# Optimization experiments

Measured on AMD Instinct MI355X. Metric: run time of the kernel, lower is better.

## Reference

```python
import math
import jax, jax.numpy as jnp
import numpy as np

B, S, D, H = 2, 2048, 1024, 16
HD = D // H

def setup_inputs() -> dict:
    key = jax.random.key(0)
    ks = jax.random.split(key, 5)
    scale = 1.0 / math.sqrt(D)
    return {
        "x": jax.random.normal(ks[0], (B, S, D), dtype=jnp.float32),
        "Wq": jax.random.normal(ks[1], (D, D), dtype=jnp.float32) * scale,
        "Wk": jax.random.normal(ks[2], (D, D), dtype=jnp.float32) * scale,
        "Wv": jax.random.normal(ks[3], (D, D), dtype=jnp.float32) * scale,
        "Wo": jax.random.normal(ks[4], (D, D), dtype=jnp.float32) * scale,
    }

def reference(x, Wq, Wk, Wv, Wo):
    b, s, d = x.shape
    # projections -> (b, h, s, hd)
    def split_heads(t):
        return t.reshape(b, s, H, HD).transpose(0, 2, 1, 3)
    q = split_heads(x @ Wq.T)
    k = split_heads(x @ Wk.T)
    v = split_heads(x @ Wv.T)
    scores = jnp.einsum('bhqd,bhkd->bhqk', q, k) / math.sqrt(HD)
    causal = jnp.tril(jnp.ones((s, s), dtype=bool))
    scores = jnp.where(causal, scores, -jnp.inf)
    weights = jax.nn.softmax(scores, axis=-1)
    attended = jnp.einsum('bhqk,bhkd->bhqd', weights, v)
    attended = attended.transpose(0, 2, 1, 3).reshape(b, s, d)
    return attended @ Wo.T
```

## Files before the change

kernel.cpp:

```cpp
#include <hip/hip_runtime.h>
#include <hip/hip_bf16.h>

#define Bb 2
#define Ss 2048
#define Dd 1024
#define Hh 16
#define HDd 64
#define Mm (Bb*Ss)

typedef __attribute__((ext_vector_type(8))) short short8;
typedef __attribute__((ext_vector_type(4))) float f32x4;

__device__ __forceinline__ unsigned short f2bf(float f) {
  unsigned int u = __float_as_uint(f);
  return (unsigned short)((u + 0x7FFFu + ((u >> 16) & 1u)) >> 16);
}

__device__ __forceinline__ void gload_lds16(const unsigned short* g, unsigned short* l) {
  __builtin_amdgcn_global_load_lds(
      (const __attribute__((address_space(1))) unsigned int*)g,
      (__attribute__((address_space(3))) unsigned int*)l, 16, 0, 0);
}

template<int ROWS>
__device__ __forceinline__ void stage_tile(const unsigned short* __restrict__ g, size_t ldg,
                                           unsigned short* s, int w, int lane) {
#pragma unroll
  for (int i = 0; i < ROWS / 32; ++i) {
    int c = (i * 4 + w) * 64 + lane;
    int row = c >> 3;
    int srcci = (lane & 7) ^ (row & 7);
    gload_lds16(g + (size_t)row * ldg + (srcci << 3), s + (i * 4 + w) * 512);
  }
}

__global__ __launch_bounds__(256) void cvt_all(
    const float* __restrict__ x,  const float* __restrict__ Wq,
    const float* __restrict__ Wk, const float* __restrict__ Wv,
    const float* __restrict__ Wo,
    unsigned short* __restrict__ xb, unsigned short* __restrict__ Wb,
    unsigned short* __restrict__ Wob) {
  int bid = blockIdx.x;
  const float* src; unsigned short* dst; int base;
  if (bid < 4096)      { src = x;  dst = xb;              base = bid; }
  else if (bid < 5120) { src = Wq; dst = Wb;              base = bid - 4096; }
  else if (bid < 6144) { src = Wk; dst = Wb + Dd * Dd;    base = bid - 5120; }
  else if (bid < 7168) { src = Wv; dst = Wb + 2 * Dd * Dd; base = bid - 6144; }
  else                 { src = Wo; dst = Wob;             base = bid - 7168; }
  int i = base * 256 + threadIdx.x;
  f32x4 v = ((const f32x4*)src)[i];
  ushort4 o;
  o.x = f2bf(v[0]); o.y = f2bf(v[1]); o.z = f2bf(v[2]); o.w = f2bf(v[3]);
  ((ushort4*)dst)[i] = o;
}

__global__ __launch_bounds__(256, 2) void gemm_qkv2(
    const unsigned short* __restrict__ xb,
    const unsigned short* __restrict__ Wb,
    unsigned short* __restrict__ Qo,
    unsigned short* __restrict__ Ko,
    unsigned short* __restrict__ Vt) {
  __shared__ unsigned short As[2][128 * 64], Bs[2][128 * 64];
  const int lin = (int)blockIdx.x + 32 * ((int)blockIdx.y + 8 * (int)blockIdx.z);
  const int orig = (lin & 7) * 96 + (lin >> 3);
  const int z = orig >> 8;
  const int rem = orig & 255;
  const int tm = (rem >> 3) * 128, tn = (rem & 7) * 128;
  const unsigned short* W = Wb + (size_t)z * Dd * Dd;
  const int tid = threadIdx.x, w = tid >> 6, lane = tid & 63;
  const int lrow = lane & 15, lgr = lane >> 4;
  const int wm = w >> 1, wn = w & 1;

  f32x4 acc[4][4] = {};
  stage_tile<128>(xb + (size_t)tm * Dd, Dd, As[0], w, lane);
  stage_tile<128>(W + (size_t)tn * Dd, Dd, Bs[0], w, lane);
  __syncthreads();
  for (int k = 0; k < 16; ++k) {
    const int cur = k & 1;
    if (k + 1 < 16) {
      stage_tile<128>(xb + (size_t)tm * Dd + (k + 1) * 64, Dd, As[cur ^ 1], w, lane);
      stage_tile<128>(W + (size_t)tn * Dd + (k + 1) * 64, Dd, Bs[cur ^ 1], w, lane);
    }
#pragma unroll
    for (int half = 0; half < 2; ++half) {
      short8 af[4], bf[4];
#pragma unroll
      for (int mt = 0; mt < 4; ++mt) {
        int row = wm * 64 + mt * 16 + lrow;
        int e = (row * 64 + half * 32 + 8 * lgr) ^ ((row & 7) << 3);
        af[mt] = *(const short8*)(As[cur] + e);
      }
#pragma unroll
      for (int nt = 0; nt < 4; ++nt) {
        int row = wn * 64 + nt * 16 + lrow;
        int e = (row * 64 + half * 32 + 8 * lgr) ^ ((row & 7) << 3);
        bf[nt] = *(const short8*)(Bs[cur] + e);
      }
      if (z != 2) {
#pragma unroll
        for (int mt = 0; mt < 4; ++mt)
#pragma unroll
          for (int nt = 0; nt < 4; ++nt)
            acc[mt][nt] = __builtin_amdgcn_mfma_f32_16x16x32_bf16(af[mt], bf[nt], acc[mt][nt], 0, 0, 0);
      } else {
#pragma unroll
        for (int mt = 0; mt < 4; ++mt)
#pragma unroll
          for (int nt = 0; nt < 4; ++nt)
            acc[mt][nt] = __builtin_amdgcn_mfma_f32_16x16x32_bf16(bf[nt], af[mt], acc[mt][nt], 0, 0, 0);
      }
    }
    __syncthreads();
  }

  unsigned short* BB = &As[0][0];
  const int brow = lane & 15, bseg = lane >> 4;
  if (z < 2) {
    unsigned short* C = z ? Ko : Qo;
#pragma unroll
    for (int mt = 0; mt < 4; ++mt) {
      unsigned short* bl = BB + (w * 2 + (mt & 1)) * (16 * 72);
#pragma unroll
      for (int nt = 0; nt < 4; ++nt)
#pragma unroll
        for (int r = 0; r < 4; ++r)
          bl[(lgr * 4 + r) * 72 + nt * 16 + lrow] = f2bf(acc[mt][nt][r]);
#pragma unroll
      for (int p = 0; p < 2; ++p) {
        short8 v = *(const short8*)(bl + brow * 72 + bseg * 8 + p * 32);
        *(short8*)(C + (size_t)(tm + wm * 64 + mt * 16 + brow) * Dd
                     + tn + wn * 64 + bseg * 8 + p * 32) = v;
      }
    }
  } else {
    const int bidx = tm >> 11;
#pragma unroll
    for (int nt = 0; nt < 4; ++nt) {
      unsigned short* bl = BB + (w * 2 + (nt & 1)) * (16 * 72);
#pragma unroll
      for (int mt = 0; mt < 4; ++mt)
#pragma unroll
        for (int r = 0; r < 4; ++r)
          bl[(lgr * 4 + r) * 72 + mt * 16 + lrow] = f2bf(acc[mt][nt][r]);
      int n = tn + wn * 64 + nt * 16 + brow;
      int h = n >> 6, hd = n & (HDd - 1);
#pragma unroll
      for (int p = 0; p < 2; ++p) {
        short8 v = *(const short8*)(bl + brow * 72 + bseg * 8 + p * 32);
        int sbase = (tm & (Ss - 1)) + wm * 64 + bseg * 8 + p * 32;
        *(short8*)(Vt + ((size_t)(bidx * Hh + h) * HDd + hd) * Ss + sbase) = v;
      }
    }
  }
}

#define SC2 0.18033688011f
__global__ __launch_bounds__(256) void attn6(
    const unsigned short* __restrict__ Q,
    const unsigned short* __restrict__ K,
    const unsigned short* __restrict__ Vt,
    unsigned short* __restrict__ att) {
  __shared__ unsigned short Ks[2][64 * 64];
  __shared__ unsigned short Vs[2][64 * 64];
  __shared__ unsigned short Ps[4][16 * 64];

  const int lin = (int)blockIdx.x + 16 * (int)blockIdx.y;
  const int orig = (lin & 7) * 64 + (lin >> 3);
  const int bhp = orig >> 4, up = orig & 15;
  const int b = bhp >> 4, h = bhp & (Hh - 1);
  const int tid = threadIdx.x, w = tid >> 6, lane = tid & 63;
  const int lrow = lane & 15, lgr = lane >> 4;

  const unsigned short* Kbase = K + (size_t)(b * Ss) * Dd + h * HDd;
  const unsigned short* Vbase = Vt + (size_t)(b * Hh + h) * HDd * Ss;
  const short8 vones = {0x3F80, 0x3F80, 0x3F80, 0x3F80, 0x3F80, 0x3F80, 0x3F80, 0x3F80};

  for (int ph = 0; ph < 2; ++ph) {
    const int qb = ph ? (31 - up) : up;
    const int qbase = qb * 64 + w * 16;
    const int nkv = qb + 1;

    const unsigned short* qp = Q + (size_t)(b * Ss + qbase + lrow) * Dd + h * HDd + 8 * lgr;
    short8 aq0 = *(const short8*)qp;
    short8 aq1 = *(const short8*)(qp + 32);

    f32x4 pacc[4] = {};
    f32x4 lacc = {};

    stage_tile<64>(Kbase, Dd, Ks[0], w, lane);
    stage_tile<64>(Vbase, Ss, Vs[0], w, lane);
    __syncthreads();

    for (int kvb = 0; kvb < nkv; ++kvb) {
      const int cur = kvb & 1;
      if (kvb + 1 < nkv) {
        stage_tile<64>(Kbase + (size_t)(kvb + 1) * 64 * Dd, Dd, Ks[cur ^ 1], w, lane);
        stage_tile<64>(Vbase + (size_t)(kvb + 1) * 64, Ss, Vs[cur ^ 1], w, lane);
      }
      f32x4 sacc[4] = {};
      __builtin_amdgcn_s_setprio(1);
#pragma unroll
      for (int nt = 0; nt < 4; ++nt) {
        int row = nt * 16 + lrow;
        int e0 = (row * 64 + 8 * lgr) ^ ((row & 7) << 3);
        int e1 = (row * 64 + 32 + 8 * lgr) ^ ((row & 7) << 3);
        short8 bk0 = *(const short8*)(Ks[cur] + e0);
        short8 bk1 = *(const short8*)(Ks[cur] + e1);
        sacc[nt] = __builtin_amdgcn_mfma_f32_16x16x32_bf16(aq0, bk0, sacc[nt], 0, 0, 0);
        sacc[nt] = __builtin_amdgcn_mfma_f32_16x16x32_bf16(aq1, bk1, sacc[nt], 0, 0, 0);
      }
      __builtin_amdgcn_s_setprio(0);
      if (kvb < qb) {
#pragma unroll
        for (int nt = 0; nt < 4; ++nt)
#pragma unroll
          for (int r = 0; r < 4; ++r)
            sacc[nt][r] = __builtin_amdgcn_exp2f(sacc[nt][r] * SC2);
      } else {
#pragma unroll
        for (int r = 0; r < 4; ++r) {
          int qg = qbase + lgr * 4 + r;
#pragma unroll
          for (int nt = 0; nt < 4; ++nt) {
            int kg = kvb * 64 + nt * 16 + lrow;
            float tt = sacc[nt][r] * SC2;
            sacc[nt][r] = (kg <= qg) ? __builtin_amdgcn_exp2f(tt) : 0.f;
          }
        }
      }
      unsigned short* pl = Ps[w];
#pragma unroll
      for (int nt = 0; nt < 4; ++nt)
#pragma unroll
        for (int r = 0; r < 4; ++r) {
          int row = lgr * 4 + r, col = nt * 16 + lrow;
          int byteoff = (row * 128 + col * 2) ^ ((row & 7) << 4);
          *(unsigned short*)((char*)pl + byteoff) =
              (unsigned short)(__float_as_uint(sacc[nt][r]) >> 16);
        }
      short8 apv[2];
#pragma unroll
      for (int ks = 0; ks < 2; ++ks) {
        int byteoff = (lrow * 128 + (ks * 32 + 8 * lgr) * 2) ^ ((lrow & 7) << 4);
        apv[ks] = *(const short8*)((char*)pl + byteoff);
      }
      __builtin_amdgcn_s_setprio(1);
#pragma unroll
      for (int nt = 0; nt < 4; ++nt) {
        int row = nt * 16 + lrow;
        int e0 = (row * 64 + 8 * lgr) ^ ((row & 7) << 3);
        int e1 = (row * 64 + 32 + 8 * lgr) ^ ((row & 7) << 3);
        short8 bv0 = *(const short8*)(Vs[cur] + e0);
        short8 bv1 = *(const short8*)(Vs[cur] + e1);
        pacc[nt] = __builtin_amdgcn_mfma_f32_16x16x32_bf16(apv[0], bv0, pacc[nt], 0, 0, 0);
        pacc[nt] = __builtin_amdgcn_mfma_f32_16x16x32_bf16(apv[1], bv1, pacc[nt], 0, 0, 0);
      }
      lacc = __builtin_amdgcn_mfma_f32_16x16x32_bf16(apv[0], vones, lacc, 0, 0, 0);
      lacc = __builtin_amdgcn_mfma_f32_16x16x32_bf16(apv[1], vones, lacc, 0, 0, 0);
      __builtin_amdgcn_s_setprio(0);
      __syncthreads();
    }
    float inv[4];
#pragma unroll
    for (int r = 0; r < 4; ++r) inv[r] = 1.f / lacc[r];
#pragma unroll
    for (int nt = 0; nt < 4; ++nt)
#pragma unroll
      for (int r = 0; r < 4; ++r) {
        int qg = qbase + lgr * 4 + r;
        att[(size_t)(b * Ss + qg) * Dd + h * HDd + nt * 16 + lrow] = f2bf(pacc[nt][r] * inv[r]);
      }
    __syncthreads();
  }
}

__global__ __launch_bounds__(256, 3) void gemm_o2(
    const unsigned short* __restrict__ att,
    const unsigned short* __restrict__ Wob,
    float* __restrict__ out) {
  __shared__ unsigned short As[2][128 * 64], Bs[2][64 * 64];
  const int lin = (int)blockIdx.x + 32 * (int)blockIdx.y;
  const int orig = (lin & 7) * 64 + (lin >> 3);
  const int tm = (orig >> 4) * 128, tn = (orig & 15) * 64;
  const int tid = threadIdx.x, w = tid >> 6, lane = tid & 63;
  const int lrow = lane & 15, lgr = lane >> 4;
  const int wm = w >> 1, wn = w & 1;

  f32x4 acc[4][2] = {};
  stage_tile<128>(att + (size_t)tm * Dd, Dd, As[0], w, lane);
  stage_tile<64>(Wob + (size_t)tn * Dd, Dd, Bs[0], w, lane);
  __syncthreads();
  for (int k = 0; k < 16; ++k) {
    const int cur = k & 1;
    if (k + 1 < 16) {
      stage_tile<128>(att + (size_t)tm * Dd + (k + 1) * 64, Dd, As[cur ^ 1], w, lane);
      stage_tile<64>(Wob + (size_t)tn * Dd + (k + 1) * 64, Dd, Bs[cur ^ 1], w, lane);
    }
#pragma unroll
    for (int half = 0; half < 2; ++half) {
      short8 af[4], bf[2];
#pragma unroll
      for (int mt = 0; mt < 4; ++mt) {
        int row = wm * 64 + mt * 16 + lrow;
        int e = (row * 64 + half * 32 + 8 * lgr) ^ ((row & 7) << 3);
        af[mt] = *(const short8*)(As[cur] + e);
      }
#pragma unroll
      for (int nt = 0; nt < 2; ++nt) {
        int row = wn * 32 + nt * 16 + lrow;
        int e = (row * 64 + half * 32 + 8 * lgr) ^ ((row & 7) << 3);
        bf[nt] = *(const short8*)(Bs[cur] + e);
      }
#pragma unroll
      for (int mt = 0; mt < 4; ++mt)
#pragma unroll
        for (int nt = 0; nt < 2; ++nt)
          acc[mt][nt] = __builtin_amdgcn_mfma_f32_16x16x32_bf16(af[mt], bf[nt], acc[mt][nt], 0, 0, 0);
    }
    __syncthreads();
  }
  const int brow = lane & 15, bseg = lane >> 4;
#pragma unroll
  for (int mt = 0; mt < 4; ++mt) {
    float* blf = ((float*)&As[0][0]) + (w * 2 + (mt & 1)) * (16 * 36);
#pragma unroll
    for (int nt = 0; nt < 2; ++nt)
#pragma unroll
      for (int r = 0; r < 4; ++r)
        blf[(lgr * 4 + r) * 36 + nt * 16 + lrow] = acc[mt][nt][r];
#pragma unroll
    for (int p = 0; p < 2; ++p) {
      f32x4 v = *(const f32x4*)(blf + brow * 36 + bseg * 4 + p * 16);
      *(f32x4*)(out + (size_t)(tm + wm * 64 + mt * 16 + brow) * Dd
                   + tn + wn * 32 + bseg * 4 + p * 16) = v;
    }
  }
}

extern "C" void kernel_launch(void* const* d_in, const int* in_sizes, int n_in,
                              void* d_out, int out_size, void* d_ws, size_t ws_size,
                              hipStream_t stream) {
  const float* x  = (const float*)d_in[0];
  const float* Wq = (const float*)d_in[1];
  const float* Wk = (const float*)d_in[2];
  const float* Wv = (const float*)d_in[3];
  const float* Wo = (const float*)d_in[4];

  char* ws = (char*)d_ws;
  unsigned short* xb  = (unsigned short*)(ws);
  unsigned short* Wb  = (unsigned short*)(ws + (8u  << 20));
  unsigned short* Wob = (unsigned short*)(ws + (14u << 20));
  unsigned short* Qb  = (unsigned short*)(ws + (16u << 20));
  unsigned short* Kb  = (unsigned short*)(ws + (24u << 20));
  unsigned short* Vt  = (unsigned short*)(ws + (32u << 20));
  unsigned short* att = xb;

  cvt_all<<<8192, 256, 0, stream>>>(x, Wq, Wk, Wv, Wo, xb, Wb, Wob);
  gemm_qkv2<<<dim3(Mm / 128, Dd / 128, 3), 256, 0, stream>>>(xb, Wb, Qb, Kb, Vt);
  attn6<<<dim3(16, 32), 256, 0, stream>>>(Qb, Kb, Vt, att);
  gemm_o2<<<dim3(Mm / 128, Dd / 64), 256, 0, stream>>>(att, Wob, (float*)d_out);
}
```

Baseline: 183.0 us.

## Pack two attention pipelines per 512-thread block; single-buffer QKV GEMM

New measurement: 226.0 us. 23.5% more time.

```diff
diff --git a/kernel.cpp b/kernel.cpp
--- a/kernel.cpp
+++ b/kernel.cpp
@@ -10,21 +10,22 @@
 
 typedef __attribute__((ext_vector_type(8))) short short8;
 typedef __attribute__((ext_vector_type(4))) float f32x4;
-
-__device__ __forceinline__ unsigned short f2bf(float f) {
+typedef unsigned short u16;
+
+__device__ __forceinline__ u16 f2bf(float f) {
   unsigned int u = __float_as_uint(f);
-  return (unsigned short)((u + 0x7FFFu + ((u >> 16) & 1u)) >> 16);
-}
-
-__device__ __forceinline__ void gload_lds16(const unsigned short* g, unsigned short* l) {
+  return (u16)((u + 0x7FFFu + ((u >> 16) & 1u)) >> 16);
+}
+
+__device__ __forceinline__ void gload_lds16(const u16* g, u16* l) {
   __builtin_amdgcn_global_load_lds(
       (const __attribute__((address_space(1))) unsigned int*)g,
       (__attribute__((address_space(3))) unsigned int*)l, 16, 0, 0);
 }
 
 template<int ROWS>
-__device__ __forceinline__ void stage_tile(const unsigned short* __restrict__ g, size_t ldg,
-                                           unsigned short* s, int w, int lane) {
+__device__ __forceinline__ void stage_tile(const u16* __restrict__ g, size_t ldg,
+                                           u16* s, int w, int lane) {
 #pragma unroll
   for (int i = 0; i < ROWS / 32; ++i) {
     int c = (i * 4 + w) * 64 + lane;
@@ -38,10 +39,9 @@
     const float* __restrict__ x,  const float* __restrict__ Wq,
     const float* __restrict__ Wk, const float* __restrict__ Wv,
     const float* __restrict__ Wo,
-    unsigned short* __restrict__ xb, unsigned short* __restrict__ Wb,
-    unsigned short* __restrict__ Wob) {
+    u16* __restrict__ xb, u16* __restrict__ Wb, u16* __restrict__ Wob) {
   int bid = blockIdx.x;
-  const float* src; unsigned short* dst; int base;
+  const float* src; u16* dst; int base;
   if (bid < 4096)      { src = x;  dst = xb;              base = bid; }
   else if (bid < 5120) { src = Wq; dst = Wb;              base = bid - 4096; }
   else if (bid < 6144) { src = Wk; dst = Wb + Dd * Dd;    base = bid - 5120; }
@@ -54,33 +54,28 @@
   ((ushort4*)dst)[i] = o;
 }
 
-__global__ __launch_bounds__(256, 2) void gemm_qkv2(
-    const unsigned short* __restrict__ xb,
-    const unsigned short* __restrict__ Wb,
-    unsigned short* __restrict__ Qo,
-    unsigned short* __restrict__ Ko,
-    unsigned short* __restrict__ Vt) {
-  __shared__ unsigned short As[2][128 * 64], Bs[2][128 * 64];
+__global__ __launch_bounds__(256, 3) void gemm_qkv2(
+    const u16* __restrict__ xb,
+    const u16* __restrict__ Wb,
+    u16* __restrict__ Qo,
+    u16* __restrict__ Ko,
+    u16* __restrict__ Vt) {
+  __shared__ u16 As[128 * 64], Bs[128 * 64];
   const int lin = (int)blockIdx.x + 32 * ((int)blockIdx.y + 8 * (int)blockIdx.z);
   const int orig = (lin & 7) * 96 + (lin >> 3);
   const int z = orig >> 8;
   const int rem = orig & 255;
   const int tm = (rem >> 3) * 128, tn = (rem & 7) * 128;
-  const unsigned short* W = Wb + (size_t)z * Dd * Dd;
+  const u16* W = Wb + (size_t)z * Dd * Dd;
   const int tid = threadIdx.x, w = tid >> 6, lane = tid & 63;
   const int lrow = lane & 15, lgr = lane >> 4;
   const int wm = w >> 1, wn = w & 1;
 
   f32x4 acc[4][4] = {};
-  stage_tile<128>(xb + (size_t)tm * Dd, Dd, As[0], w, lane);
-  stage_tile<128>(W + (size_t)tn * Dd, Dd, Bs[0], w, lane);
-  __syncthreads();
-  for (int k = 0; k < 16; ++k) {
-    const int cur = k & 1;
-    if (k + 1 < 16) {
-      stage_tile<128>(xb + (size_t)tm * Dd + (k + 1) * 64, Dd, As[cur ^ 1], w, lane);
-      stage_tile<128>(W + (size_t)tn * Dd + (k + 1) * 64, Dd, Bs[cur ^ 1], w, lane);
-    }
+  for (int k0 = 0; k0 < Dd; k0 += 64) {
+    stage_tile<128>(xb + (size_t)tm * Dd + k0, Dd, As, w, lane);
+    stage_tile<128>(W + (size_t)tn * Dd + k0, Dd, Bs, w, lane);
+    __syncthreads();
 #pragma unroll
     for (int half = 0; half < 2; ++half) {
       short8 af[4], bf[4];
@@ -88,13 +83,13 @@
       for (int mt = 0; mt < 4; ++mt) {
         int row = wm * 64 + mt * 16 + lrow;
         int e = (row * 64 + half * 32 + 8 * lgr) ^ ((row & 7) << 3);
-        af[mt] = *(const short8*)(As[cur] + e);
+        af[mt] = *(const short8*)(As + e);
       }
 #pragma unroll
       for (int nt = 0; nt < 4; ++nt) {
         int row = wn * 64 + nt * 16 + lrow;
         int e = (row * 64 + half * 32 + 8 * lgr) ^ ((row & 7) << 3);
-        bf[nt] = *(const short8*)(Bs[cur] + e);
+        bf[nt] = *(const short8*)(Bs + e);
       }
       if (z != 2) {
 #pragma unroll
@@ -113,13 +108,13 @@
     __syncthreads();
   }
 
-  unsigned short* BB = &As[0][0];
+  u16* BB = &As[0];
   const int brow = lane & 15, bseg = lane >> 4;
   if (z < 2) {
-    unsigned short* C = z ? Ko : Qo;
+    u16* C = z ? Ko : Qo;
 #pragma unroll
     for (int mt = 0; mt < 4; ++mt) {
-      unsigned short* bl = BB + (w * 2 + (mt & 1)) * (16 * 72);
+      u16* bl = BB + (w * 2 + (mt & 1)) * (16 * 72);
 #pragma unroll
       for (int nt = 0; nt < 4; ++nt)
 #pragma unroll
@@ -136,7 +131,7 @@
     const int bidx = tm >> 11;
 #pragma unroll
     for (int nt = 0; nt < 4; ++nt) {
-      unsigned short* bl = BB + (w * 2 + (nt & 1)) * (16 * 72);
+      u16* bl = BB + (w * 2 + (nt & 1)) * (16 * 72);
 #pragma unroll
       for (int mt = 0; mt < 4; ++mt)
 #pragma unroll
@@ -155,47 +150,53 @@
 }
 
 #define SC2 0.18033688011f
-__global__ __launch_bounds__(256) void attn6(
-    const unsigned short* __restrict__ Q,
-    const unsigned short* __restrict__ K,
-    const unsigned short* __restrict__ Vt,
-    unsigned short* __restrict__ att) {
-  __shared__ unsigned short Ks[2][64 * 64];
-  __shared__ unsigned short Vs[2][64 * 64];
-  __shared__ unsigned short Ps[4][16 * 64];
-
-  const int lin = (int)blockIdx.x + 16 * (int)blockIdx.y;
-  const int orig = (lin & 7) * 64 + (lin >> 3);
-  const int bhp = orig >> 4, up = orig & 15;
-  const int b = bhp >> 4, h = bhp & (Hh - 1);
+__global__ __launch_bounds__(512) void attn7(
+    const u16* __restrict__ Q,
+    const u16* __restrict__ K,
+    const u16* __restrict__ Vt,
+    u16* __restrict__ att) {
+  __shared__ u16 KsAll[2][2][64 * 64];
+  __shared__ u16 VsAll[2][2][64 * 64];
+  __shared__ u16 PsAll[2][4][16 * 64];
+
+  const int lin = (int)blockIdx.x + 8 * (int)blockIdx.y;
+  const int orig = (lin & 7) * 32 + (lin >> 3);
+  const int bh = orig >> 3, ublock = orig & 7;
+  const int b = bh >> 4, h = bh & (Hh - 1);
   const int tid = threadIdx.x, w = tid >> 6, lane = tid & 63;
+  const int pipe = w >> 2, w4 = w & 3;
+  const int up = ublock + 8 * pipe;
   const int lrow = lane & 15, lgr = lane >> 4;
 
-  const unsigned short* Kbase = K + (size_t)(b * Ss) * Dd + h * HDd;
-  const unsigned short* Vbase = Vt + (size_t)(b * Hh + h) * HDd * Ss;
+  u16 (*Ks)[64 * 64] = KsAll[pipe];
+  u16 (*Vs)[64 * 64] = VsAll[pipe];
+  u16* pl = PsAll[pipe][w4];
+
+  const u16* Kbase = K + (size_t)(b * Ss) * Dd + h * HDd;
+  const u16* Vbase = Vt + (size_t)(b * Hh + h) * HDd * Ss;
   const short8 vones = {0x3F80, 0x3F80, 0x3F80, 0x3F80, 0x3F80, 0x3F80, 0x3F80, 0x3F80};
 
   for (int ph = 0; ph < 2; ++ph) {
     const int qb = ph ? (31 - up) : up;
-    const int qbase = qb * 64 + w * 16;
+    const int qbase = qb * 64 + w4 * 16;
     const int nkv = qb + 1;
 
-    const unsigned short* qp = Q + (size_t)(b * Ss + qbase + lrow) * Dd + h * HDd + 8 * lgr;
+    const u16* qp = Q + (size_t)(b * Ss + qbase + lrow) * Dd + h * HDd + 8 * lgr;
     short8 aq0 = *(const short8*)qp;
     short8 aq1 = *(const short8*)(qp + 32);
 
     f32x4 pacc[4] = {};
     f32x4 lacc = {};
 
-    stage_tile<64>(Kbase, Dd, Ks[0], w, lane);
-    stage_tile<64>(Vbase, Ss, Vs[0], w, lane);
+    stage_tile<64>(Kbase, Dd, Ks[0], w4, lane);
+    stage_tile<64>(Vbase, Ss, Vs[0], w4, lane);
     __syncthreads();
 
     for (int kvb = 0; kvb < nkv; ++kvb) {
       const int cur = kvb & 1;
       if (kvb + 1 < nkv) {
-        stage_tile<64>(Kbase + (size_t)(kvb + 1) * 64 * Dd, Dd, Ks[cur ^ 1], w, lane);
-        stage_tile<64>(Vbase + (size_t)(kvb + 1) * 64, Ss, Vs[cur ^ 1], w, lane);
+        stage_tile<64>(Kbase + (size_t)(kvb + 1) * 64 * Dd, Dd, Ks[cur ^ 1], w4, lane);
+        stage_tile<64>(Vbase + (size_t)(kvb + 1) * 64, Ss, Vs[cur ^ 1], w4, lane);
       }
       f32x4 sacc[4] = {};
       __builtin_amdgcn_s_setprio(1);
@@ -228,15 +229,14 @@
           }
         }
       }
-      unsigned short* pl = Ps[w];
 #pragma unroll
       for (int nt = 0; nt < 4; ++nt)
 #pragma unroll
         for (int r = 0; r < 4; ++r) {
           int row = lgr * 4 + r, col = nt * 16 + lrow;
           int byteoff = (row * 128 + col * 2) ^ ((row & 7) << 4);
-          *(unsigned short*)((char*)pl + byteoff) =
-              (unsigned short)(__float_as_uint(sacc[nt][r]) >> 16);
+          *(u16*)((char*)pl + byteoff) =
+              (u16)(__float_as_uint(sacc[nt][r]) >> 16);
         }
       short8 apv[2];
 #pragma unroll
@@ -275,10 +275,10 @@
 }
 
 __global__ __launch_bounds__(256, 3) void gemm_o2(
-    const unsigned short* __restrict__ att,
-    const unsigned short* __restrict__ Wob,
+    const u16* __restrict__ att,
+    const u16* __restrict__ Wob,
     float* __restrict__ out) {
-  __shared__ unsigned short As[2][128 * 64], Bs[2][64 * 64];
+  __shared__ u16 As[2][128 * 64], Bs[2][64 * 64];
   const int lin = (int)blockIdx.x + 32 * (int)blockIdx.y;
   const int orig = (lin & 7) * 64 + (lin >> 3);
   const int tm = (orig >> 4) * 128, tn = (orig & 15) * 64;
@@ -347,16 +347,16 @@
   const float* Wo = (const float*)d_in[4];
 
   char* ws = (char*)d_ws;
-  unsigned short* xb  = (unsigned short*)(ws);
-  unsigned short* Wb  = (unsigned short*)(ws + (8u  << 20));
-  unsigned short* Wob = (unsigned short*)(ws + (14u << 20));
-  unsigned short* Qb  = (unsigned short*)(ws + (16u << 20));
-  unsigned short* Kb  = (unsigned short*)(ws + (24u << 20));
-  unsigned short* Vt  = (unsigned short*)(ws + (32u << 20));
-  unsigned short* att = xb;
+  u16* xb  = (u16*)(ws);
+  u16* Wb  = (u16*)(ws + (8u  << 20));
+  u16* Wob = (u16*)(ws + (14u << 20));
+  u16* Qb  = (u16*)(ws + (16u << 20));
+  u16* Kb  = (u16*)(ws + (24u << 20));
+  u16* Vt  = (u16*)(ws + (32u << 20));
+  u16* att = xb;
 
   cvt_all<<<8192, 256, 0, stream>>>(x, Wq, Wk, Wv, Wo, xb, Wb, Wob);
   gemm_qkv2<<<dim3(Mm / 128, Dd / 128, 3), 256, 0, stream>>>(xb, Wb, Qb, Kb, Vt);
-  attn6<<<dim3(16, 32), 256, 0, stream>>>(Qb, Kb, Vt, att);
+  attn7<<<dim3(8, 32), 512, 0, stream>>>(Qb, Kb, Vt, att);
   gemm_o2<<<dim3(Mm / 128, Dd / 64), 256, 0, stream>>>(att, Wob, (float*)d_out);
 }
```
